# Kernel tuning notes

Hardware: AMD Instinct MI355X
Metric: run time of the kernel (lower is better)

## Reference

```python
import jax, jax.numpy as jnp
import numpy as np

NH = 8          # attention heads
NC = 14         # disease classes
K = 10          # aspect queries per class
E = 1024        # vision_dim == text_dim
HID = 512       # hidden_dim = vision_dim // 2
TEMP = 0.1
LN_EPS = 1e-5


def _layernorm(x, g, b):
    m = jnp.mean(x, axis=-1, keepdims=True)
    v = jnp.mean(jnp.square(x - m), axis=-1, keepdims=True)
    return (x - m) * jax.lax.rsqrt(v + LN_EPS) * g + b


def _mha(q, k, v, in_w, in_b, out_w, out_b):
    # nn.MultiheadAttention (batch_first, eval mode => dropout off)
    B, Lq, Emb = q.shape
    Lk = k.shape[1]
    dh = Emb // NH
    wq, wk, wv = jnp.split(in_w, 3, axis=0)
    bq, bk, bv = jnp.split(in_b, 3)
    qh = (q @ wq.T + bq).reshape(B, Lq, NH, dh)
    kh = (k @ wk.T + bk).reshape(B, Lk, NH, dh)
    vh = (v @ wv.T + bv).reshape(B, Lk, NH, dh)
    scale = np.float32(1.0 / np.sqrt(dh))
    scores = jnp.einsum('bqhd,bkhd->bhqk', qh, kh) * scale
    attn = jax.nn.softmax(scores, axis=-1)
    out = jnp.einsum('bhqk,bkhd->bqhd', attn, vh).reshape(B, Lq, Emb)
    out = out @ out_w.T + out_b
    return out, attn.mean(axis=1)  # avg over heads, (B, Lq, Lk)


def _l2norm(x):
    return x / jnp.maximum(jnp.linalg.norm(x, axis=-1, keepdims=True), 1e-12)


def reference(vision_features, text_embeddings, vision_global, aspect_queries,
              ch_in_w, ch_in_b, ch_out_w, ch_out_b, tp_w, tp_b,
              ca_in_w, ca_in_b, ca_out_w, ca_out_b,
              cross_ln_g, cross_ln_b, cross_fc_w, cross_fc_b,
              dir_ln_g, dir_ln_b, dir_w1, dir_b1, dir_w2, dir_b2):
    B, N, _ = vision_features.shape
    # ---- contrastive branch (1-token query / 1-token kv attention) ----
    text_proj = text_embeddings @ tp_w.T + tp_b               # (B, E)
    c_out, _ = _mha(vision_global[:, None, :], text_proj[:, None, :],
                    text_proj[:, None, :], ch_in_w, ch_in_b, ch_out_w, ch_out_b)
    sim = jnp.sum(_l2norm(c_out[:, 0, :]) * _l2norm(text_proj), axis=-1) / TEMP  # (B,)
    contrastive_logits = jnp.broadcast_to(sim[:, None], (B, NC))
    # ---- supervised branch: fused per-class cross-attention (shared K/V) ----
    q = jnp.broadcast_to(aspect_queries.reshape(1, NC * K, E), (B, NC * K, E))
    att_out, attn_w = _mha(q, vision_features, vision_features,
                           ca_in_w, ca_in_b, ca_out_w, ca_out_b)
    attended = att_out.reshape(B, NC, K, E).mean(axis=2)       # (B, NC, E)
    attention_weights = attn_w.reshape(B, NC, K, N)            # (B, NC, K, N)
    # fc_cross: LN + per-class linear row (class j feature -> class j logit)
    h = _layernorm(attended, cross_ln_g, cross_ln_b)
    logits_cross = jnp.einsum('bjd,jd->bj', h, cross_fc_w) + cross_fc_b
    # fc_direct MLP on global feature
    g = _layernorm(vision_global, dir_ln_g, dir_ln_b)
    logits_direct = jax.nn.relu(g @ dir_w1.T + dir_b1) @ dir_w2.T + dir_b2
    supervised_logits = (logits_cross + logits_direct) * 0.5
    final_logits = (supervised_logits + contrastive_logits) * 0.5
    return contrastive_logits, supervised_logits, final_logits, attention_weights


def setup_inputs() -> dict:
    key = jax.random.key(0)
    ks = jax.random.split(key, 16)
    B, N = 64, 576
    w = lambda k, s: (jax.random.normal(k, s, dtype=jnp.float32) * 0.02)
    return {
        'vision_features': jax.random.normal(ks[0], (B, N, E), dtype=jnp.float32),
        'text_embeddings': jax.random.normal(ks[1], (B, E), dtype=jnp.float32),
        'vision_global': jax.random.normal(ks[2], (B, E), dtype=jnp.float32),
        'aspect_queries': jax.random.normal(ks[3], (NC, K, E), dtype=jnp.float32) / np.sqrt(E).astype(np.float32),
        'ch_in_w': w(ks[4], (3 * E, E)), 'ch_in_b': jnp.zeros((3 * E,), jnp.float32),
        'ch_out_w': w(ks[5], (E, E)), 'ch_out_b': jnp.zeros((E,), jnp.float32),
        'tp_w': w(ks[6], (E, E)), 'tp_b': jnp.zeros((E,), jnp.float32),
        'ca_in_w': w(ks[7], (3 * E, E)), 'ca_in_b': jnp.zeros((3 * E,), jnp.float32),
        'ca_out_w': w(ks[8], (E, E)), 'ca_out_b': jnp.zeros((E,), jnp.float32),
        'cross_ln_g': jnp.ones((E,), jnp.float32), 'cross_ln_b': jnp.zeros((E,), jnp.float32),
        'cross_fc_w': w(ks[9], (NC, E)), 'cross_fc_b': jnp.zeros((NC,), jnp.float32),
        'dir_ln_g': jnp.ones((E,), jnp.float32), 'dir_ln_b': jnp.zeros((E,), jnp.float32),
        'dir_w1': w(ks[10], (HID, E)), 'dir_b1': jnp.zeros((HID,), jnp.float32),
        'dir_w2': w(ks[11], (NC, HID)), 'dir_b2': jnp.zeros((NC,), jnp.float32),
    }
```

## Files before the change

### kernel.cpp

```cpp
#include <hip/hip_runtime.h>
#include <cstdio>
#include <cstdint>

using u16 = unsigned short;
typedef __bf16 bf16x8 __attribute__((ext_vector_type(8)));
typedef float f32x4 __attribute__((ext_vector_type(4)));

#define GLOBAL_AS __attribute__((address_space(1)))
#define LDS_AS __attribute__((address_space(3)))

__device__ __forceinline__ float bf2f(u16 h) {
  return __uint_as_float(((unsigned)h) << 16);
}
__device__ __forceinline__ u16 f2bf(float f) {
  unsigned u = __float_as_uint(f);
  u += 0x7FFFu + ((u >> 16) & 1u);
  return (u16)(u >> 16);
}

__device__ __forceinline__ void async_copy16(void* lds, const void* g) {
  __builtin_amdgcn_global_load_lds((const GLOBAL_AS unsigned int*)g,
                                   (LDS_AS unsigned int*)lds, 16, 0, 0);
}

__device__ __forceinline__ float block_sum(float v, float* red) {
#pragma unroll
  for (int o = 32; o >= 1; o >>= 1) v += __shfl_xor(v, o);
  __syncthreads();
  if ((threadIdx.x & 63) == 0) red[threadIdx.x >> 6] = v;
  __syncthreads();
  return red[0] + red[1] + red[2] + red[3];
}
__device__ __forceinline__ float block_max(float v, float* red) {
#pragma unroll
  for (int o = 32; o >= 1; o >>= 1) v = fmaxf(v, __shfl_xor(v, o));
  __syncthreads();
  if ((threadIdx.x & 63) == 0) red[threadIdx.x >> 6] = v;
  __syncthreads();
  return fmaxf(fmaxf(red[0], red[1]), fmaxf(red[2], red[3]));
}

__global__ __launch_bounds__(256) void cvt4_kernel(
    const float* __restrict__ s0, u16* __restrict__ d0,
    const float* __restrict__ s1, u16* __restrict__ d1,
    const float* __restrict__ s2, u16* __restrict__ d2,
    const float* __restrict__ s3, u16* __restrict__ d3) {
  const float* s; u16* d; long n; long b0; long nb;
  const int b = blockIdx.x;
  if (b < 2048)      { s = s0; d = d0; n = 37748736L; b0 = b;        nb = 2048; }
  else if (b < 2816) { s = s1; d = d1; n = 3145728L;  b0 = b - 2048; nb = 768; }
  else if (b < 3072) { s = s2; d = d2; n = 1048576L;  b0 = b - 2816; nb = 256; }
  else               { s = s3; d = d3; n = 143360L;   b0 = b - 3072; nb = 35; }
  long i = (b0 * 256 + threadIdx.x) * 4;
  const long stride = nb * 1024;
  for (; i < n; i += stride) {
    float4 v = *(const float4*)(s + i);
    ushort4 o;
    o.x = f2bf(v.x); o.y = f2bf(v.y); o.z = f2bf(v.z); o.w = f2bf(v.w);
    *(ushort4*)(d + i) = o;
  }
}

template <int VTD>
__global__ __launch_bounds__(512, 2) void gemm_kvq_kernel(
    const u16* __restrict__ A, const u16* __restrict__ Bkv,
    const u16* __restrict__ Aq, const u16* __restrict__ Bq,
    u16* __restrict__ Ck, u16* __restrict__ Cvp, u16* __restrict__ Vt,
    u16* __restrict__ Cq,
    const float* __restrict__ bias, const float* __restrict__ biasq) {
  __shared__ u16 lds[3][24576];
  const int bid = blockIdx.x;
  const int t = threadIdx.x;
  const int wid = t >> 6, l = t & 63;
  const int wr = wid >> 1, wc = wid & 1;
  const int lr = l & 15, lg = l >> 4, lr7 = lr & 7;

  int mt = 0, nt = 0, qb = -1;
  const u16* Abase; const u16* Bbase; const float* bias_b;
  if (bid < 2304) {
    const int wgid = (bid & 7) * 288 + (bid >> 3);
    mt = wgid >> 4; nt = wgid & 15;
    Abase = A + (size_t)mt * 256 * 1024;
    Bbase = Bkv + (size_t)nt * 128 * 1024;
    bias_b = bias + nt * 128;
  } else {
    qb = bid - 2304;
    Abase = Aq;
    Bbase = Bq + (size_t)qb * 128 * 1024;
    bias_b = biasq + qb * 128;
  }

  const int srow = t >> 3;
  const int scx = (t & 7) ^ (srow & 7);
  const char* Asrc = (const char*)Abase + (size_t)srow * 2048 + (scx << 4);
  const char* Bsrc = (const char*)Bbase + (size_t)srow * 2048 + (scx << 4);
  const int wbA = wid << 10;

  char* b0 = (char*)lds[0];
  char* b1 = (char*)lds[1];
  char* b2 = (char*)lds[2];

  f32x4 acc[4][4] = {};

#define STAGE3(dst, kt, part)                                               \
  {                                                                         \
    const size_t ko = (size_t)(kt) * 128;                                   \
    if ((part) == 0) {                                                      \
      async_copy16((dst) + wbA,          Asrc + ko);                        \
      async_copy16((dst) + 8192 + wbA,   Asrc + 131072 + ko);               \
      async_copy16((dst) + 16384 + wbA,  Asrc + 262144 + ko);               \
    } else {                                                                \
      async_copy16((dst) + 24576 + wbA,  Asrc + 393216 + ko);               \
      async_copy16((dst) + 32768 + wbA,  Bsrc + ko);                        \
      async_copy16((dst) + 40960 + wbA,  Bsrc + 131072 + ko);               \
    }                                                                       \
  }

#define COMPUTE_KS(p, KS)                                                   \
  {                                                                         \
    const int ccol = (((KS) << 2) | lg) ^ lr7;                              \
    const char* pA = (p) + (((wr << 6) + lr) << 7) + (ccol << 4);           \
    const char* pB = (p) + 32768 + (((wc << 6) + lr) << 7) + (ccol << 4);   \
    bf16x8 af[4], bfr[4];                                                   \
    _Pragma("unroll")                                                       \
    for (int i = 0; i < 4; ++i) {                                           \
      af[i]  = *(const bf16x8*)(pA + i * 2048);                             \
      bfr[i] = *(const bf16x8*)(pB + i * 2048);                             \
    }                                                                       \
    __builtin_amdgcn_s_setprio(1);                                          \
    _Pragma("unroll")                                                       \
    for (int mi = 0; mi < 4; ++mi)                                          \
      _Pragma("unroll")                                                     \
      for (int ni = 0; ni < 4; ++ni)                                        \
        acc[mi][ni] = __builtin_amdgcn_mfma_f32_16x16x32_bf16(              \
            af[mi], bfr[ni], acc[mi][ni], 0, 0, 0);                         \
    __builtin_amdgcn_s_setprio(0);                                          \
  }

  STAGE3(b0, 0, 0); STAGE3(b0, 0, 1);
  STAGE3(b1, 1, 0); STAGE3(b1, 1, 1);
  asm volatile("s_waitcnt vmcnt(6)" ::: "memory");
  __builtin_amdgcn_s_barrier();
  asm volatile("" ::: "memory");

  char* p0 = b0; char* p1 = b1; char* p2 = b2;
#pragma unroll 1
  for (int kt = 0; kt < 16; ++kt) {
    const bool pf = (kt < 14);
    if (pf) STAGE3(p2, kt + 2, 0);
    COMPUTE_KS(p0, 0);
    if (pf) STAGE3(p2, kt + 2, 1);
    COMPUTE_KS(p0, 1);
    if (kt < 15) {
      if (pf) asm volatile("s_waitcnt vmcnt(6)" ::: "memory");
      else    asm volatile("s_waitcnt vmcnt(0)" ::: "memory");
      __builtin_amdgcn_s_barrier();
      asm volatile("" ::: "memory");
    }
    char* tmp = p0; p0 = p1; p1 = p2; p2 = tmp;
  }
#undef STAGE3
#undef COMPUTE_KS

  const int mrow0 = wr * 64 + lg * 4;
  if (VTD && qb < 0 && nt >= 8) {
    const int n0 = (nt - 8) * 128 + wc * 64;
#pragma unroll
    for (int ni = 0; ni < 4; ++ni) {
      const int n = n0 + ni * 16 + lr;
      const int h = n >> 7, d = n & 127;
      const float bv = bias_b[wc * 64 + ni * 16 + lr];
      u16* vh = Vt + ((size_t)h * 128 + d) * 576;
#pragma unroll
      for (int mi = 0; mi < 4; ++mi) {
#pragma unroll
        for (int rg = 0; rg < 4; ++rg) {
          const int m = mt * 256 + mrow0 + mi * 16 + rg;
          const int b = (unsigned)m / 576u;
          const int k = m - b * 576;
          vh[(size_t)b * 589824 + k] = f2bf(acc[mi][ni][rg] + bv);
        }
      }
    }
  } else {
    u16* Cb;
    if (qb >= 0)      Cb = Cq + (size_t)qb * 128;
    else if (nt < 8)  Cb = Ck + (size_t)nt * 128 + (size_t)mt * 256 * 1024;
    else              Cb = Cvp + (size_t)(nt - 8) * 128 + (size_t)mt * 256 * 1024;
#pragma unroll
    for (int ni = 0; ni < 4; ++ni) {
      const int nc = wc * 64 + ni * 16 + lr;
      const float bv = bias_b[nc];
#pragma unroll
      for (int mi = 0; mi < 4; ++mi) {
#pragma unroll
        for (int rg = 0; rg < 4; ++rg) {
          const size_t m = (size_t)(mrow0 + mi * 16 + rg);
          Cb[m * 1024 + nc] = f2bf(acc[mi][ni][rg] + bv);
        }
      }
    }
  }
}

template <int OUTF32>
__global__ __launch_bounds__(256) void gemm_bt_kernel(
    const u16* __restrict__ A, const u16* __restrict__ B, void* __restrict__ Cv,
    const float* __restrict__ bias, float scale,
    int M, int N, int K, int lda, int ldb, int ldc,
    int ntiles, int bdiv,
    long sA0, long sA1, long sB0, long sB1, long sC0, long sC1) {
  __shared__ u16 Alds[128 * 64];
  __shared__ u16 Blds[128 * 64];
  const int bh = blockIdx.y;
  const int b0 = bh / bdiv, b1 = bh % bdiv;
  const int tile = blockIdx.x;
  const long mt0 = (long)(tile / ntiles) * 128;
  const long nt0 = (long)(tile % ntiles) * 128;
  const int t = threadIdx.x;
  const int w = t >> 6, l = t & 63;
  const int wm = (w >> 1) * 64, wn = (w & 1) * 64;
  const int srow = l >> 3;
  const int scol = l & 7;
  const long ldab = (long)lda * 2, ldbb = (long)ldb * 2;
  const char* Abase = (const char*)(A + b0 * sA0 + b1 * sA1) + mt0 * ldab;
  const char* Bbase = (const char*)(B + b0 * sB0 + b1 * sB1) + nt0 * ldbb;

  f32x4 acc[4][4] = {};

  for (int kk = 0; kk < K; kk += 64) {
    const char* Ak = Abase + (long)kk * 2;
    const char* Bk = Bbase + (long)kk * 2;
#pragma unroll
    for (int r = 0; r < 4; ++r) {
      const int row0 = r * 32 + w * 8;
      async_copy16((char*)Alds + row0 * 128, Ak + (long)(row0 + srow) * ldab + scol * 16);
      async_copy16((char*)Blds + row0 * 128, Bk + (long)(row0 + srow) * ldbb + scol * 16);
    }
    asm volatile("s_waitcnt vmcnt(0)" ::: "memory");
    __syncthreads();
#pragma unroll
    for (int ks = 0; ks < 2; ++ks) {
      bf16x8 af[4], bfr[4];
#pragma unroll
      for (int i = 0; i < 4; ++i) {
        const int ra = wm + i * 16 + (l & 15);
        const int ca = ks * 4 + (l >> 4);
        af[i] = *(const bf16x8*)((const char*)Alds + ra * 128 + ca * 16);
        const int rb = wn + i * 16 + (l & 15);
        bfr[i] = *(const bf16x8*)((const char*)Blds + rb * 128 + ca * 16);
      }
#pragma unroll
      for (int mi = 0; mi < 4; ++mi)
#pragma unroll
        for (int ni = 0; ni < 4; ++ni)
          acc[mi][ni] = __builtin_amdgcn_mfma_f32_16x16x32_bf16(af[mi], bfr[ni], acc[mi][ni], 0, 0, 0);
    }
    __syncthreads();
  }

  const long cBase = (long)b0 * sC0 + (long)b1 * sC1;
  const int mr0 = (int)mt0 + wm + (l >> 4) * 4;
  const int nc0 = (int)nt0 + wn + (l & 15);
#pragma unroll
  for (int ni = 0; ni < 4; ++ni) {
    const int n = nc0 + ni * 16;
    if (n >= N) continue;
    const float bv = bias ? bias[n] : 0.0f;
#pragma unroll
    for (int mi = 0; mi < 4; ++mi) {
#pragma unroll
      for (int rg = 0; rg < 4; ++rg) {
        const int m = mr0 + mi * 16 + rg;
        if (m >= M) continue;
        const float v = acc[mi][ni][rg] * scale + bv;
        if (OUTF32) ((float*)Cv)[cBase + (long)m * ldc + n] = v;
        else        ((u16*)Cv)[cBase + (long)m * ldc + n] = f2bf(v);
      }
    }
  }
}

__global__ __launch_bounds__(256) void transpose_v_kernel(const u16* __restrict__ V,
                                                          u16* __restrict__ Vt) {
  __shared__ u16 tile[64][65];
  const int k0 = blockIdx.x * 64;
  const int c0 = blockIdx.y * 64;
  const int b = blockIdx.z;
  const int t = threadIdx.x;
  const int tx = t & 15, ty = t >> 4;
  const u16* Vb = V + (size_t)(b * 576) * 1024;
#pragma unroll
  for (int i = 0; i < 4; ++i) {
    const int k = ty + i * 16;
    const u16* src = Vb + (size_t)(k0 + k) * 1024 + c0 + tx * 4;
    ushort2 v01 = *(const ushort2*)src;
    ushort2 v23 = *(const ushort2*)(src + 2);
    tile[k][tx * 4 + 0] = v01.x; tile[k][tx * 4 + 1] = v01.y;
    tile[k][tx * 4 + 2] = v23.x; tile[k][tx * 4 + 3] = v23.y;
  }
  __syncthreads();
  const int h = c0 >> 7, d0 = c0 & 127;
  u16* VtB = Vt + ((size_t)(b * 8 + h) * 128 + d0) * 576 + k0;
#pragma unroll
  for (int i = 0; i < 4; ++i) {
    const int d = ty + i * 16;
    u16* dst = VtB + (size_t)d * 576 + tx * 4;
    ushort2 a, bb2;
    a.x = tile[tx * 4 + 0][d]; a.y = tile[tx * 4 + 1][d];
    bb2.x = tile[tx * 4 + 2][d]; bb2.y = tile[tx * 4 + 3][d];
    *(ushort2*)dst = a; *(ushort2*)(dst + 2) = bb2;
  }
}

__global__ __launch_bounds__(512) void softmax_attn_kernel(u16* __restrict__ SP,
                                                           float* __restrict__ attnOut) {
  const int b = blockIdx.x, q = blockIdx.y;
  const int h = threadIdx.x >> 6, l = threadIdx.x & 63;
  __shared__ float pl[8][576];
  u16* row = SP + ((size_t)((b * 8 + h) * 144 + q)) * 576;
  float x[9];
#pragma unroll
  for (int i = 0; i < 9; ++i) x[i] = bf2f(row[l + 64 * i]);
  float m = x[0];
#pragma unroll
  for (int i = 1; i < 9; ++i) m = fmaxf(m, x[i]);
#pragma unroll
  for (int o = 32; o >= 1; o >>= 1) m = fmaxf(m, __shfl_xor(m, o));
  float e[9], s = 0.f;
#pragma unroll
  for (int i = 0; i < 9; ++i) { e[i] = expf(x[i] - m); s += e[i]; }
#pragma unroll
  for (int o = 32; o >= 1; o >>= 1) s += __shfl_xor(s, o);
  const float inv = 1.f / s;
#pragma unroll
  for (int i = 0; i < 9; ++i) {
    const float p = e[i] * inv;
    row[l + 64 * i] = f2bf(p);
    pl[h][l + 64 * i] = p;
  }
  __syncthreads();
  float* out = attnOut + ((size_t)(b * 140 + q)) * 576;
  for (int j = threadIdx.x; j < 576; j += 512) {
    float a = 0.f;
#pragma unroll
    for (int hh = 0; hh < 8; ++hh) a += pl[hh][j];
    out[j] = a * 0.125f;
  }
}

__global__ __launch_bounds__(256) void mean_o_kernel(const float* __restrict__ O,
                                                     u16* __restrict__ attended) {
  const int bc = blockIdx.x;
  const int b = bc / 14, c = bc % 14;
  const int t = threadIdx.x;
  const float* base = O + ((size_t)b * 140 + c * 10) * 1024;
#pragma unroll
  for (int i = 0; i < 4; ++i) {
    const int e = t + i * 256;
    float s = 0.f;
#pragma unroll
    for (int j = 0; j < 10; ++j) s += base[(size_t)j * 1024 + e];
    attended[(size_t)bc * 1024 + e] = f2bf(s * 0.1f);
  }
}

__global__ __launch_bounds__(256) void ln_crossfc_kernel(
    const float* __restrict__ ap, const float* __restrict__ g, const float* __restrict__ bb,
    const float* __restrict__ fw, const float* __restrict__ fb, float* __restrict__ out) {
  const int bc = blockIdx.x;
  const int c = bc % 14;
  const float* x = ap + (size_t)bc * 1024;
  __shared__ float red[4];
  const int t = threadIdx.x;
  float v[4];
  float s = 0.f;
#pragma unroll
  for (int i = 0; i < 4; ++i) { v[i] = x[t + i * 256]; s += v[i]; }
  const float mean = block_sum(s, red) * (1.f / 1024.f);
  float vs = 0.f;
#pragma unroll
  for (int i = 0; i < 4; ++i) { const float d = v[i] - mean; vs += d * d; }
  const float var = block_sum(vs, red) * (1.f / 1024.f);
  const float inv = rsqrtf(var + 1e-5f);
  float acc = 0.f;
#pragma unroll
  for (int i = 0; i < 4; ++i) {
    const int e = t + i * 256;
    const float h = (v[i] - mean) * inv * g[e] + bb[e];
    acc += h * fw[(size_t)c * 1024 + e];
  }
  acc = block_sum(acc, red);
  if (t == 0) out[bc] = acc + fb[c];
}

__global__ __launch_bounds__(256) void direct_mlp_kernel(
    const float* __restrict__ vg, const float* __restrict__ g, const float* __restrict__ bb,
    const float* __restrict__ w1, const float* __restrict__ b1,
    const float* __restrict__ w2, const float* __restrict__ b2, float* __restrict__ out) {
  const int b = blockIdx.x;
  __shared__ float red[4];
  __shared__ float gn[1024];
  __shared__ float h1[512];
  const int t = threadIdx.x;
  const float* x = vg + (size_t)b * 1024;
  float v[4];
  float s = 0.f;
#pragma unroll
  for (int i = 0; i < 4; ++i) { v[i] = x[t + i * 256]; s += v[i]; }
  const float mean = block_sum(s, red) * (1.f / 1024.f);
  float vs = 0.f;
#pragma unroll
  for (int i = 0; i < 4; ++i) { const float d = v[i] - mean; vs += d * d; }
  const float var = block_sum(vs, red) * (1.f / 1024.f);
  const float inv = rsqrtf(var + 1e-5f);
#pragma unroll
  for (int i = 0; i < 4; ++i) {
    const int e = t + i * 256;
    gn[e] = (v[i] - mean) * inv * g[e] + bb[e];
  }
  __syncthreads();
  for (int j = t; j < 512; j += 256) {
    float a = b1[j];
    const float4* wr = (const float4*)(w1 + (size_t)j * 1024);
    const float4* g4 = (const float4*)gn;
    for (int e = 0; e < 256; ++e) {
      float4 wv = wr[e], av = g4[e];
      a += av.x * wv.x + av.y * wv.y + av.z * wv.z + av.w * wv.w;
    }
    h1[j] = fmaxf(a, 0.f);
  }
  __syncthreads();
  for (int c = 0; c < 14; ++c) {
    float a = 0.f;
    for (int j = t; j < 512; j += 256) a += h1[j] * w2[(size_t)c * 512 + j];
    a = block_sum(a, red);
    if (t == 0) out[b * 14 + c] = a + b2[c];
  }
}

__global__ __launch_bounds__(256) void linear_f32_kernel(
    const float* __restrict__ A, const float* __restrict__ W, const float* __restrict__ bias,
    float* __restrict__ C, int N, int Kd) {
  const int r = blockIdx.x;
  const int j = blockIdx.y * 256 + threadIdx.x;
  __shared__ float a[1024];
  for (int e = threadIdx.x; e < Kd; e += 256) a[e] = A[(size_t)r * Kd + e];
  __syncthreads();
  float acc = bias ? bias[j] : 0.f;
  const float4* wr = (const float4*)(W + (size_t)j * Kd);
  const float4* a4 = (const float4*)a;
  for (int e = 0; e < Kd / 4; ++e) {
    float4 wv = wr[e], av = a4[e];
    acc += av.x * wv.x + av.y * wv.y + av.z * wv.z + av.w * wv.w;
  }
  C[(size_t)r * N + j] = acc;
}

__global__ __launch_bounds__(256) void sim_kernel(const float* __restrict__ co,
                                                  const float* __restrict__ tp,
                                                  float* __restrict__ sim) {
  const int b = blockIdx.x;
  const int t = threadIdx.x;
  __shared__ float red[4];
  const float* c = co + (size_t)b * 1024;
  const float* p = tp + (size_t)b * 1024;
  float dd = 0.f, nc = 0.f, nt = 0.f;
  for (int e = t; e < 1024; e += 256) {
    const float cv = c[e], pv = p[e];
    dd += cv * pv; nc += cv * cv; nt += pv * pv;
  }
  dd = block_sum(dd, red);
  nc = block_sum(nc, red);
  nt = block_sum(nt, red);
  if (t == 0)
    sim[b] = dd / (fmaxf(sqrtf(nc), 1e-12f) * fmaxf(sqrtf(nt), 1e-12f)) / 0.1f;
}

__global__ __launch_bounds__(256) void combine_kernel(const float* __restrict__ sim,
                                                      const float* __restrict__ lc,
                                                      const float* __restrict__ ld,
                                                      float* __restrict__ out) {
  const int i = blockIdx.x * 256 + threadIdx.x;
  if (i >= 896) return;
  const int b = i / 14;
  const float contr = sim[b];
  const float sup = 0.5f * (lc[i] + ld[i]);
  const float fin = 0.5f * (sup + contr);
  out[i] = contr;
  out[896 + i] = sup;
  out[1792 + i] = fin;
}

static constexpr size_t OFF_X    = 0;
static constexpr size_t OFF_K    = OFF_X + 75497472;
static constexpr size_t OFF_SP   = OFF_K + 75759616;
static constexpr size_t OFF_WIN  = OFF_SP + 85082112;
static constexpr size_t OFF_WOUT = OFF_WIN + 6291456;
static constexpr size_t OFF_ASP  = OFF_WOUT + 2097152;
static constexpr size_t OFF_QASP = OFF_ASP + 524288;
static constexpr size_t OFF_ATT  = OFF_QASP + 524288;
static constexpr size_t OFF_APRJ = OFF_ATT + 1835008;
static constexpr size_t OFF_TP   = OFF_APRJ + 3670016;
static constexpr size_t OFF_CV   = OFF_TP + 262144;
static constexpr size_t OFF_CO   = OFF_CV + 262144;
static constexpr size_t OFF_SIM  = OFF_CO + 262144;
static constexpr size_t OFF_LC   = OFF_SIM + 4096;
static constexpr size_t OFF_LD   = OFF_LC + 4096;
static constexpr size_t WS_SMALL = OFF_LD + 4096;
static constexpr size_t OFF_VT   = WS_SMALL;
static constexpr size_t WS_BIG   = OFF_VT + 75497472;

extern "C" void kernel_launch(void* const* d_in, const int* in_sizes, int n_in,
                              void* d_out, int out_size, void* d_ws, size_t ws_size,
                              hipStream_t stream) {
  (void)in_sizes; (void)n_in; (void)out_size;
  const float* vision_features = (const float*)d_in[0];
  const float* text_embeddings = (const float*)d_in[1];
  const float* vision_global   = (const float*)d_in[2];
  const float* aspect_queries  = (const float*)d_in[3];
  const float* ch_in_w  = (const float*)d_in[4];
  const float* ch_in_b  = (const float*)d_in[5];
  const float* ch_out_w = (const float*)d_in[6];
  const float* ch_out_b = (const float*)d_in[7];
  const float* tp_w = (const float*)d_in[8];
  const float* tp_b = (const float*)d_in[9];
  const float* ca_in_w  = (const float*)d_in[10];
  const float* ca_in_b  = (const float*)d_in[11];
  const float* ca_out_w = (const float*)d_in[12];
  const float* ca_out_b = (const float*)d_in[13];
  const float* cross_ln_g = (const float*)d_in[14];
  const float* cross_ln_b = (const float*)d_in[15];
  const float* cross_fc_w = (const float*)d_in[16];
  const float* cross_fc_b = (const float*)d_in[17];
  const float* dir_ln_g = (const float*)d_in[18];
  const float* dir_ln_b = (const float*)d_in[19];
  const float* dir_w1 = (const float*)d_in[20];
  const float* dir_b1 = (const float*)d_in[21];
  const float* dir_w2 = (const float*)d_in[22];
  const float* dir_b2 = (const float*)d_in[23];

  if (ws_size < WS_SMALL) {
    fprintf(stderr, "kernel_launch: ws too small: %zu < %zu\n", ws_size, WS_SMALL);
    return;
  }
  const bool big = (ws_size >= WS_BIG);

  char* ws = (char*)d_ws;
  u16* Xb      = (u16*)(ws + OFF_X);
  u16* Kb      = (u16*)(ws + OFF_K);
  float* O_all = (float*)(ws + OFF_K);
  u16* Vb      = (u16*)(ws + OFF_SP);
  u16* SP      = (u16*)(ws + OFF_SP);
  u16* Vt      = big ? (u16*)(ws + OFF_VT) : (u16*)(ws + OFF_X);
  u16* Win     = (u16*)(ws + OFF_WIN);
  u16* Wout    = (u16*)(ws + OFF_WOUT);
  u16* Asp     = (u16*)(ws + OFF_ASP);
  u16* Qasp    = (u16*)(ws + OFF_QASP);
  u16* Attd    = (u16*)(ws + OFF_ATT);
  float* Aprj  = (float*)(ws + OFF_APRJ);
  float* Tp    = (float*)(ws + OFF_TP);
  float* Cv2   = (float*)(ws + OFF_CV);
  float* Co    = (float*)(ws + OFF_CO);
  float* Sim   = (float*)(ws + OFF_SIM);
  float* Lc    = (float*)(ws + OFF_LC);
  float* Ld    = (float*)(ws + OFF_LD);
  float* attnOut = (float*)d_out + 2688;

  cvt4_kernel<<<3107, 256, 0, stream>>>(vision_features, Xb, ca_in_w, Win,
                                        ca_out_w, Wout, aspect_queries, Asp);

  if (big) {
    gemm_kvq_kernel<1><<<dim3(2312), 512, 0, stream>>>(
        Xb, Win + 1024 * 1024, Asp, Win, Kb, nullptr, Vt, Qasp,
        ca_in_b + 1024, ca_in_b);
  } else {
    gemm_kvq_kernel<0><<<dim3(2312), 512, 0, stream>>>(
        Xb, Win + 1024 * 1024, Asp, Win, Kb, Vb, nullptr, Qasp,
        ca_in_b + 1024, ca_in_b);
    transpose_v_kernel<<<dim3(9, 16, 64), 256, 0, stream>>>(Vb, Vt);
  }

  gemm_bt_kernel<0><<<dim3(2 * 5, 512), 256, 0, stream>>>(
      Qasp, Kb, SP, nullptr, 0.08838834764831845f,
      140, 576, 128, 1024, 1024, 576, 5, 8,
      0L, 128L, 589824L, 128L, 663552L, 82944L);

  softmax_attn_kernel<<<dim3(64, 140), 512, 0, stream>>>(SP, attnOut);

  gemm_bt_kernel<1><<<dim3(2 * 1, 512), 256, 0, stream>>>(
      SP, Vt, O_all, nullptr, 1.0f,
      140, 128, 576, 576, 576, 1024, 1, 8,
      663552L, 82944L, 589824L, 73728L, 143360L, 128L);

  mean_o_kernel<<<896, 256, 0, stream>>>(O_all, Attd);

  gemm_bt_kernel<1><<<dim3(7 * 8, 1), 256, 0, stream>>>(
      Attd, Wout, Aprj, ca_out_b, 1.0f,
      896, 1024, 1024, 1024, 1024, 1024, 8, 1, 0, 0, 0, 0, 0, 0);

  ln_crossfc_kernel<<<896, 256, 0, stream>>>(Aprj, cross_ln_g, cross_ln_b,
                                             cross_fc_w, cross_fc_b, Lc);

  direct_mlp_kernel<<<64, 256, 0, stream>>>(vision_global, dir_ln_g, dir_ln_b,
                                            dir_w1, dir_b1, dir_w2, dir_b2, Ld);

  linear_f32_kernel<<<dim3(64, 4), 256, 0, stream>>>(text_embeddings, tp_w, tp_b, Tp, 1024, 1024);
  linear_f32_kernel<<<dim3(64, 4), 256, 0, stream>>>(Tp, ch_in_w + 2048 * 1024, ch_in_b + 2048, Cv2, 1024, 1024);
  linear_f32_kernel<<<dim3(64, 4), 256, 0, stream>>>(Cv2, ch_out_w, ch_out_b, Co, 1024, 1024);
  sim_kernel<<<64, 256, 0, stream>>>(Co, Tp, Sim);

  combine_kernel<<<4, 256, 0, stream>>>(Sim, Lc, Ld, (float*)d_out);
}
```

Baseline: 651.0 us.

## Replace attention GEMMs with 256x128 triple-buffered swizzled kernel; stage V transpose via LDS

The generic 128x128 single-buffered bt-GEMM is replaced by a 512-thread, 256x128-tile kernel. It triple-buffers LDS with async global-to-LDS loads, XOR-swizzles columns to avoid bank conflicts, and raises MFMA priority, so loads overlap compute. It is used for QK^T, PV and the output projection. The fused V-transpose epilogue in the KVQ GEMM now stages tiles through LDS and writes coalesced 16-byte rows instead of scattered 2-byte stores. The M=140 attention GEMMs now compute a 256-row tile per batch-head, which wastes MFMA work. The 147KB LDS also limits occupancy.

```diff
diff --git a/kernel.cpp b/kernel.cpp
--- a/kernel.cpp
+++ b/kernel.cpp
@@ -30,14 +30,6 @@
   if ((threadIdx.x & 63) == 0) red[threadIdx.x >> 6] = v;
   __syncthreads();
   return red[0] + red[1] + red[2] + red[3];
-}
-__device__ __forceinline__ float block_max(float v, float* red) {
-#pragma unroll
-  for (int o = 32; o >= 1; o >>= 1) v = fmaxf(v, __shfl_xor(v, o));
-  __syncthreads();
-  if ((threadIdx.x & 63) == 0) red[threadIdx.x >> 6] = v;
-  __syncthreads();
-  return fmaxf(fmaxf(red[0], red[1]), fmaxf(red[2], red[3]));
 }
 
 __global__ __launch_bounds__(256) void cvt4_kernel(
@@ -164,24 +156,34 @@
 
   const int mrow0 = wr * 64 + lg * 4;
   if (VTD && qb < 0 && nt >= 8) {
-    const int n0 = (nt - 8) * 128 + wc * 64;
+    __syncthreads();
+    u16* T = (u16*)lds;
 #pragma unroll
     for (int ni = 0; ni < 4; ++ni) {
-      const int n = n0 + ni * 16 + lr;
-      const int h = n >> 7, d = n & 127;
-      const float bv = bias_b[wc * 64 + ni * 16 + lr];
-      u16* vh = Vt + ((size_t)h * 128 + d) * 576;
+      const int nl = wc * 64 + ni * 16 + lr;
+      const float bv = bias_b[nl];
 #pragma unroll
       for (int mi = 0; mi < 4; ++mi) {
-#pragma unroll
-        for (int rg = 0; rg < 4; ++rg) {
-          const int m = mt * 256 + mrow0 + mi * 16 + rg;
-          const int b = (unsigned)m / 576u;
-          const int k = m - b * 576;
-          vh[(size_t)b * 589824 + k] = f2bf(acc[mi][ni][rg] + bv);
-        }
+        const int ml = mrow0 + mi * 16;
+        ushort4 pk;
+        pk.x = f2bf(acc[mi][ni][0] + bv);
+        pk.y = f2bf(acc[mi][ni][1] + bv);
+        pk.z = f2bf(acc[mi][ni][2] + bv);
+        pk.w = f2bf(acc[mi][ni][3] + bv);
+        *(ushort4*)(T + (size_t)nl * 264 + ml) = pk;
       }
     }
+    __syncthreads();
+    const int n_row = t >> 2, seg = t & 3;
+    const int hh = nt - 8;
+    const int m0 = mt * 256 + seg * 64;
+    const int b = (unsigned)m0 / 576u;
+    const int k0 = m0 - b * 576;
+    u16* dst = Vt + ((size_t)(b * 8 + hh) * 128 + n_row) * 576 + k0;
+    const u16* src = T + (size_t)n_row * 264 + seg * 64;
+#pragma unroll
+    for (int i = 0; i < 8; ++i)
+      *(uint4*)(dst + i * 8) = *(const uint4*)(src + i * 8);
   } else {
     u16* Cb;
     if (qb >= 0)      Cb = Cq + (size_t)qb * 128;
@@ -204,75 +206,112 @@
 }
 
 template <int OUTF32>
-__global__ __launch_bounds__(256) void gemm_bt_kernel(
+__global__ __launch_bounds__(512, 2) void gemm_big_kernel(
     const u16* __restrict__ A, const u16* __restrict__ B, void* __restrict__ Cv,
     const float* __restrict__ bias, float scale,
-    int M, int N, int K, int lda, int ldb, int ldc,
-    int ntiles, int bdiv,
+    int KT, int ntx, int Mlim, int Nlim,
+    long lda, long ldb, long ldc, int bdiv,
     long sA0, long sA1, long sB0, long sB1, long sC0, long sC1) {
-  __shared__ u16 Alds[128 * 64];
-  __shared__ u16 Blds[128 * 64];
+  __shared__ u16 lds[3][24576];
+  const int bid = blockIdx.x;
   const int bh = blockIdx.y;
-  const int b0 = bh / bdiv, b1 = bh % bdiv;
-  const int tile = blockIdx.x;
-  const long mt0 = (long)(tile / ntiles) * 128;
-  const long nt0 = (long)(tile % ntiles) * 128;
+  const int bb0 = bh / bdiv, bb1 = bh % bdiv;
+  const int mt = bid / ntx, nt = bid % ntx;
   const int t = threadIdx.x;
-  const int w = t >> 6, l = t & 63;
-  const int wm = (w >> 1) * 64, wn = (w & 1) * 64;
-  const int srow = l >> 3;
-  const int scol = l & 7;
-  const long ldab = (long)lda * 2, ldbb = (long)ldb * 2;
-  const char* Abase = (const char*)(A + b0 * sA0 + b1 * sA1) + mt0 * ldab;
-  const char* Bbase = (const char*)(B + b0 * sB0 + b1 * sB1) + nt0 * ldbb;
+  const int wid = t >> 6, l = t & 63;
+  const int wr = wid >> 1, wc = wid & 1;
+  const int lr = l & 15, lg = l >> 4, lr7 = lr & 7;
+
+  const long ldab = lda * 2, ldbb = ldb * 2;
+  const u16* Abase = A + (long)bb0 * sA0 + (long)bb1 * sA1 + (long)mt * 256 * lda;
+  const u16* Bbase = B + (long)bb0 * sB0 + (long)bb1 * sB1 + (long)nt * 128 * ldb;
+
+  const int srow = t >> 3;
+  const int scx = (t & 7) ^ (srow & 7);
+  const char* Asrc = (const char*)Abase + (long)srow * ldab + (scx << 4);
+  const char* Bsrc = (const char*)Bbase + (long)srow * ldbb + (scx << 4);
+  const int wbA = wid << 10;
+
+  char* b0 = (char*)lds[0];
+  char* b1 = (char*)lds[1];
+  char* b2 = (char*)lds[2];
 
   f32x4 acc[4][4] = {};
 
-  for (int kk = 0; kk < K; kk += 64) {
-    const char* Ak = Abase + (long)kk * 2;
-    const char* Bk = Bbase + (long)kk * 2;
-#pragma unroll
-    for (int r = 0; r < 4; ++r) {
-      const int row0 = r * 32 + w * 8;
-      async_copy16((char*)Alds + row0 * 128, Ak + (long)(row0 + srow) * ldab + scol * 16);
-      async_copy16((char*)Blds + row0 * 128, Bk + (long)(row0 + srow) * ldbb + scol * 16);
+#define STAGE3G(dst, kt, part)                                              \
+  {                                                                         \
+    const long ko = (long)(kt) * 128;                                       \
+    if ((part) == 0) {                                                      \
+      async_copy16((dst) + wbA,          Asrc + ko);                        \
+      async_copy16((dst) + 8192 + wbA,   Asrc + 64 * ldab + ko);            \
+      async_copy16((dst) + 16384 + wbA,  Asrc + 128 * ldab + ko);           \
+    } else {                                                                \
+      async_copy16((dst) + 24576 + wbA,  Asrc + 192 * ldab + ko);           \
+      async_copy16((dst) + 32768 + wbA,  Bsrc + ko);                        \
+      async_copy16((dst) + 40960 + wbA,  Bsrc + 64 * ldbb + ko);            \
+    }                                                                       \
+  }
+
+#define COMPUTE_KS(p, KS)                                                   \
+  {                                                                         \
+    const int ccol = (((KS) << 2) | lg) ^ lr7;                              \
+    const char* pA = (p) + (((wr << 6) + lr) << 7) + (ccol << 4);           \
+    const char* pB = (p) + 32768 + (((wc << 6) + lr) << 7) + (ccol << 4);   \
+    bf16x8 af[4], bfr[4];                                                   \
+    _Pragma("unroll")                                                       \
+    for (int i = 0; i < 4; ++i) {                                           \
+      af[i]  = *(const bf16x8*)(pA + i * 2048);                             \
+      bfr[i] = *(const bf16x8*)(pB + i * 2048);                             \
+    }                                                                       \
+    __builtin_amdgcn_s_setprio(1);                                          \
+    _Pragma("unroll")                                                       \
+    for (int mi = 0; mi < 4; ++mi)                                          \
+      _Pragma("unroll")                                                     \
+      for (int ni = 0; ni < 4; ++ni)                                        \
+        acc[mi][ni] = __builtin_amdgcn_mfma_f32_16x16x32_bf16(              \
+            af[mi], bfr[ni], acc[mi][ni], 0, 0, 0);                         \
+    __builtin_amdgcn_s_setprio(0);                                          \
+  }
+
+  STAGE3G(b0, 0, 0); STAGE3G(b0, 0, 1);
+  STAGE3G(b1, 1, 0); STAGE3G(b1, 1, 1);
+  asm volatile("s_waitcnt vmcnt(6)" ::: "memory");
+  __builtin_amdgcn_s_barrier();
+  asm volatile("" ::: "memory");
+
+  char* p0 = b0; char* p1 = b1; char* p2 = b2;
+#pragma unroll 1
+  for (int kt = 0; kt < KT; ++kt) {
+    const bool pf = (kt < KT - 2);
+    if (pf) STAGE3G(p2, kt + 2, 0);
+    COMPUTE_KS(p0, 0);
+    if (pf) STAGE3G(p2, kt + 2, 1);
+    COMPUTE_KS(p0, 1);
+    if (kt < KT - 1) {
+      if (pf) asm volatile("s_waitcnt vmcnt(6)" ::: "memory");
+      else    asm volatile("s_waitcnt vmcnt(0)" ::: "memory");
+      __builtin_amdgcn_s_barrier();
+      asm volatile("" ::: "memory");
     }
-    asm volatile("s_waitcnt vmcnt(0)" ::: "memory");
-    __syncthreads();
-#pragma unroll
-    for (int ks = 0; ks < 2; ++ks) {
-      bf16x8 af[4], bfr[4];
-#pragma unroll
-      for (int i = 0; i < 4; ++i) {
-        const int ra = wm + i * 16 + (l & 15);
-        const int ca = ks * 4 + (l >> 4);
-        af[i] = *(const bf16x8*)((const char*)Alds + ra * 128 + ca * 16);
-        const int rb = wn + i * 16 + (l & 15);
-        bfr[i] = *(const bf16x8*)((const char*)Blds + rb * 128 + ca * 16);
-      }
-#pragma unroll
-      for (int mi = 0; mi < 4; ++mi)
-#pragma unroll
-        for (int ni = 0; ni < 4; ++ni)
-          acc[mi][ni] = __builtin_amdgcn_mfma_f32_16x16x32_bf16(af[mi], bfr[ni], acc[mi][ni], 0, 0, 0);
-    }
-    __syncthreads();
-  }
-
-  const long cBase = (long)b0 * sC0 + (long)b1 * sC1;
-  const int mr0 = (int)mt0 + wm + (l >> 4) * 4;
-  const int nc0 = (int)nt0 + wn + (l & 15);
+    char* tmp = p0; p0 = p1; p1 = p2; p2 = tmp;
+  }
+#undef STAGE3G
+#undef COMPUTE_KS
+
+  const long cBase = (long)bb0 * sC0 + (long)bb1 * sC1;
+  const int mr0 = mt * 256 + wr * 64 + lg * 4;
+  const int nc0 = nt * 128 + wc * 64 + lr;
 #pragma unroll
   for (int ni = 0; ni < 4; ++ni) {
     const int n = nc0 + ni * 16;
-    if (n >= N) continue;
+    if (n >= Nlim) continue;
     const float bv = bias ? bias[n] : 0.0f;
 #pragma unroll
     for (int mi = 0; mi < 4; ++mi) {
 #pragma unroll
       for (int rg = 0; rg < 4; ++rg) {
         const int m = mr0 + mi * 16 + rg;
-        if (m >= M) continue;
+        if (m >= Mlim) continue;
         const float v = acc[mi][ni][rg] * scale + bv;
         if (OUTF32) ((float*)Cv)[cBase + (long)m * ldc + n] = v;
         else        ((u16*)Cv)[cBase + (long)m * ldc + n] = f2bf(v);
@@ -581,23 +620,24 @@
     transpose_v_kernel<<<dim3(9, 16, 64), 256, 0, stream>>>(Vb, Vt);
   }
 
-  gemm_bt_kernel<0><<<dim3(2 * 5, 512), 256, 0, stream>>>(
+  gemm_big_kernel<0><<<dim3(5, 512), 512, 0, stream>>>(
       Qasp, Kb, SP, nullptr, 0.08838834764831845f,
-      140, 576, 128, 1024, 1024, 576, 5, 8,
+      2, 5, 140, 576, 1024, 1024, 576, 8,
       0L, 128L, 589824L, 128L, 663552L, 82944L);
 
   softmax_attn_kernel<<<dim3(64, 140), 512, 0, stream>>>(SP, attnOut);
 
-  gemm_bt_kernel<1><<<dim3(2 * 1, 512), 256, 0, stream>>>(
+  gemm_big_kernel<1><<<dim3(1, 512), 512, 0, stream>>>(
       SP, Vt, O_all, nullptr, 1.0f,
-      140, 128, 576, 576, 576, 1024, 1, 8,
+      9, 1, 140, 128, 576, 576, 1024, 8,
       663552L, 82944L, 589824L, 73728L, 143360L, 128L);
 
   mean_o_kernel<<<896, 256, 0, stream>>>(O_all, Attd);
 
-  gemm_bt_kernel<1><<<dim3(7 * 8, 1), 256, 0, stream>>>(
+  gemm_big_kernel<1><<<dim3(32, 1), 512, 0, stream>>>(
       Attd, Wout, Aprj, ca_out_b, 1.0f,
-      896, 1024, 1024, 1024, 1024, 1024, 8, 1, 0, 0, 0, 0, 0, 0);
+      16, 8, 896, 1024, 1024, 1024, 1024, 1,
+      0L, 0L, 0L, 0L, 0L, 0L);
 
   ln_crossfc_kernel<<<896, 256, 0, stream>>>(Aprj, cross_ln_g, cross_ln_b,
                                              cross_fc_w, cross_fc_b, Lc);
```

Measured after the change: 646.4 us. About the same (-0.7%).
